# Performance work log

Hardware: AMD Instinct MI355X
Metric: run time of the kernel (lower is better)

Reference implementation:

```python
import jax, jax.numpy as jnp
import numpy as np

E = 16      # num_experts
H = 1024    # hidden_size
O = 1       # output_size
B = 4096    # batch
K = 2       # top-k (hard-coded in module)


def setup_inputs() -> dict:
    key = jax.random.key(0)
    ks = jax.random.split(key, 7)
    s_h = 1.0 / np.sqrt(H)
    inp = {
        "embeddings": jax.random.normal(ks[0], (B, H), dtype=jnp.float32),
        "router_w": jax.random.uniform(ks[1], (H, E), jnp.float32, -s_h, s_h),
        "router_b": jax.random.uniform(ks[2], (E,), jnp.float32, -s_h, s_h),
        "w1": jax.random.uniform(ks[3], (E, H, H), jnp.float32, -s_h, s_h),
        "b1": jax.random.uniform(ks[4], (E, H), jnp.float32, -s_h, s_h),
        "w2": jax.random.uniform(ks[5], (E, H, O), jnp.float32, -s_h, s_h),
        "b2": jax.random.uniform(ks[6], (E, O), jnp.float32, -s_h, s_h),
    }
    return inp


def reference(embeddings, router_w, router_b, w1, b1, w2, b2):
    # Router: top-2 experts per token, softmax over the 2 selected logits.
    logits = embeddings @ router_w + router_b                 # [B, E]
    top_vals, top_idx = jax.lax.top_k(logits, K)              # [B, K]
    top_w = jax.nn.softmax(top_vals, axis=-1)                 # [B, K]

    # Per-expert combine weight: w_e[b] = sum_k top_w[b,k] * (top_idx[b,k]==e)
    onehot = (top_idx[:, :, None] == jnp.arange(E)[None, None, :])  # [B, K, E]
    comb = jnp.einsum('bk,bke->eb', top_w, onehot.astype(top_w.dtype))  # [E, B]

    # Dense per-expert 2-layer MLP (small fixed E); masked-weighted combine
    # reproduces the gather/scatter-add exactly.
    h = jax.nn.relu(jnp.einsum('bh,ehd->ebd', embeddings, w1) + b1[:, None, :])  # [E, B, H]
    out = jnp.einsum('ebd,edo->ebo', h, w2) + b2[:, None, :]                      # [E, B, O]
    prediction = jnp.einsum('eb,ebo->bo', comb, out)                              # [B, O]
    return prediction
```

## Files before the change

kernel.cpp:

```cpp
#include <hip/hip_runtime.h>
#include <hip/hip_bf16.h>
#include <stdint.h>

#define E_EXP 16
#define H_DIM 1024
#define B_TOK 4096
#define BK 64
#define WBM 64
#define WBN 64
#define NSLOT 16
#define KS 16
#define KC 64
#define RTM 128
#define RSTRIDE (KC + 4)

typedef short bf16x8 __attribute__((ext_vector_type(8)));
typedef float f32x4 __attribute__((ext_vector_type(4)));

__device__ __forceinline__ unsigned short f2bf(float x) {
  union { float f; unsigned u; } v; v.f = x;
  unsigned r = v.u + 0x7FFFu + ((v.u >> 16) & 1u);
  return (unsigned short)(r >> 16);
}

__device__ __forceinline__ void gload_lds16(const void* g, void* l) {
  __builtin_amdgcn_global_load_lds(
      (const __attribute__((address_space(1))) void*)g,
      (__attribute__((address_space(3))) void*)l, 16, 0, 0);
}

__global__ __launch_bounds__(256) void k_prep(
    const float* __restrict__ emb, const float* __restrict__ rw,
    const float* __restrict__ w1, unsigned short* __restrict__ emb_bf,
    float* __restrict__ part, unsigned short* __restrict__ w1t,
    int* __restrict__ counts)
{
  __shared__ __align__(16) char smem[RTM * RSTRIDE * 4 + KC * E_EXP * 4];
  const int tid = threadIdx.x;

  if (blockIdx.x == 0 && tid < E_EXP) counts[tid] = 0;

  if (blockIdx.x < 512) {
    float* embL = (float*)smem;
    float* rwL  = (float*)(smem + RTM * RSTRIDE * 4);
    const int t0 = (blockIdx.x & 31) * RTM;
    const int ks = blockIdx.x >> 5;

#pragma unroll
    for (int it = 0; it < 8; ++it) {
      const int i = tid + 256 * it;
      const int row = i >> 4;
      const int c4 = i & 15;
      const size_t goff = (size_t)(t0 + row) * H_DIM + ks * KC + c4 * 4;
      const f32x4 v = *(const f32x4*)(emb + goff);
      ushort4 o;
      o.x = f2bf(v[0]); o.y = f2bf(v[1]); o.z = f2bf(v[2]); o.w = f2bf(v[3]);
      *(ushort4*)(emb_bf + goff) = o;
      *(f32x4*)(embL + row * RSTRIDE + c4 * 4) = v;
    }
    {
      const f32x4 v = *(const f32x4*)(rw + (size_t)ks * (KC * E_EXP) + tid * 4);
      *(f32x4*)(rwL + tid * 4) = v;
    }
    __syncthreads();

    const int w = tid >> 6, lane = tid & 63;
    const int tg = lane & 15, eg = lane >> 4;
    const int ta = w * 32 + tg, tb = ta + 16;

    f32x4 accA = {0.f, 0.f, 0.f, 0.f};
    f32x4 accB = {0.f, 0.f, 0.f, 0.f};
#pragma unroll
    for (int k4 = 0; k4 < KC / 4; ++k4) {
      const f32x4 e0 = *(const f32x4*)(embL + ta * RSTRIDE + k4 * 4);
      const f32x4 e1 = *(const f32x4*)(embL + tb * RSTRIDE + k4 * 4);
#pragma unroll
      for (int h = 0; h < 4; ++h) {
        const f32x4 r = *(const f32x4*)(rwL + (k4 * 4 + h) * E_EXP + eg * 4);
        accA += e0[h] * r;
        accB += e1[h] * r;
      }
    }
    *(f32x4*)(part + ((size_t)ks * B_TOK + t0 + ta) * E_EXP + eg * 4) = accA;
    *(f32x4*)(part + ((size_t)ks * B_TOK + t0 + tb) * E_EXP + eg * 4) = accB;
  } else {
    typedef unsigned short TileT[65];
    TileT* tile = (TileT*)smem;
    const int wb = blockIdx.x - 512;
    const int e  = wb >> 8;
    const int ht = (wb >> 4) & 15;
    const int dt = wb & 15;
    const float* src = w1 + ((size_t)e * H_DIM + ht * 64) * H_DIM + dt * 64;
    const int tr = tid >> 4;
    const int tc = tid & 15;
#pragma unroll
    for (int i = 0; i < 4; ++i) {
      const int r = tr + i * 16;
      const float4 v = *(const float4*)(src + (size_t)r * H_DIM + tc * 4);
      tile[r][tc * 4 + 0] = f2bf(v.x);
      tile[r][tc * 4 + 1] = f2bf(v.y);
      tile[r][tc * 4 + 2] = f2bf(v.z);
      tile[r][tc * 4 + 3] = f2bf(v.w);
    }
    __syncthreads();
    unsigned short* dst = w1t + ((size_t)e * H_DIM + dt * 64) * H_DIM + ht * 64;
    const int wr = tid >> 3;
    const int wc = tid & 7;
#pragma unroll
    for (int i = 0; i < 2; ++i) {
      const int r = wr + i * 32;
      ushort4 t0, t1;
      t0.x = tile[wc * 8 + 0][r]; t0.y = tile[wc * 8 + 1][r];
      t0.z = tile[wc * 8 + 2][r]; t0.w = tile[wc * 8 + 3][r];
      t1.x = tile[wc * 8 + 4][r]; t1.y = tile[wc * 8 + 5][r];
      t1.z = tile[wc * 8 + 6][r]; t1.w = tile[wc * 8 + 7][r];
      *(ushort4*)(dst + (size_t)r * H_DIM + wc * 8) = t0;
      *(ushort4*)(dst + (size_t)r * H_DIM + wc * 8 + 4) = t1;
    }
  }
}

__global__ __launch_bounds__(256) void k_router_select(
    const float* __restrict__ part, const float* __restrict__ rb,
    int* __restrict__ counts, int* __restrict__ lists,
    int4* __restrict__ meta, float2* __restrict__ wts)
{
  __shared__ int lcnt[E_EXP];
  __shared__ int base[E_EXP];
  const int tid = threadIdx.x;
  const int t = blockIdx.x * 256 + tid;
  if (tid < E_EXP) lcnt[tid] = 0;

  float lg[16];
#pragma unroll
  for (int q = 0; q < 4; ++q) {
    const f32x4 b = *(const f32x4*)(rb + q * 4);
    lg[q * 4 + 0] = b[0]; lg[q * 4 + 1] = b[1];
    lg[q * 4 + 2] = b[2]; lg[q * 4 + 3] = b[3];
  }
#pragma unroll
  for (int s = 0; s < KS; ++s) {
#pragma unroll
    for (int q = 0; q < 4; ++q) {
      const f32x4 v = *(const f32x4*)(part + ((size_t)s * B_TOK + t) * E_EXP + q * 4);
      lg[q * 4 + 0] += v[0]; lg[q * 4 + 1] += v[1];
      lg[q * 4 + 2] += v[2]; lg[q * 4 + 3] += v[3];
    }
  }

  float best = -1e30f; int b0 = 0;
#pragma unroll
  for (int e = 0; e < 16; ++e)
    if (lg[e] > best) { best = lg[e]; b0 = e; }
  float best2 = -1e30f; int b1i = 0;
#pragma unroll
  for (int e = 0; e < 16; ++e)
    if (e != b0 && lg[e] > best2) { best2 = lg[e]; b1i = e; }

  __syncthreads();
  const int l0 = atomicAdd(&lcnt[b0], 1);
  const int l1 = atomicAdd(&lcnt[b1i], 1);
  __syncthreads();
  if (tid < E_EXP) base[tid] = atomicAdd(&counts[tid], lcnt[tid]);
  __syncthreads();

  const int p0 = base[b0] + l0;
  const int p1 = base[b1i] + l1;
  lists[b0 * B_TOK + p0] = t;
  lists[b1i * B_TOK + p1] = t;
  meta[t] = make_int4(b0, b1i, p0, p1);
  const float e1v = expf(best2 - best);
  const float w0 = 1.f / (1.f + e1v);
  wts[t] = make_float2(w0, e1v * w0);
}

__global__ __launch_bounds__(64) void k_moe_gemm(
    const unsigned short* __restrict__ emb_bf,
    const unsigned short* __restrict__ w1t,
    const float* __restrict__ b1, const float* __restrict__ w2,
    const int* __restrict__ counts, const int* __restrict__ lists,
    float* __restrict__ outbuf)
{
  const int bid = blockIdx.x;
  const int xcd = bid & 7;
  const int j = bid >> 3;
  const int e  = xcd + 8 * (j >> 8);
  const int r  = j & 255;
  const int nb = r >> 4;
  const int mbg = r & 15;
  const int cnt = counts[e];

  __shared__ unsigned short lA[WBM * BK];
  __shared__ unsigned short lB[WBN * BK];

  const int lane = threadIdx.x;
  const int scb = ((lane & 7) * 16) ^ ((lane >> 3) << 4);
  const int lr = lane & 15, lg = lane >> 4;

  const unsigned short* w1tb = w1t + ((size_t)e * H_DIM + nb * WBN) * H_DIM;
  const float* b1e = b1 + (size_t)e * H_DIM + nb * WBN;
  const float* w2e = w2 + (size_t)e * H_DIM + nb * WBN;

  const unsigned short* bSrc[8];
#pragma unroll
  for (int i = 0; i < 8; ++i) {
    const int n = i * 8 + (lane >> 3);
    bSrc[i] = w1tb + (size_t)n * H_DIM + (scb >> 1);
  }

  for (int mb = mbg; mb * WBM < cnt; mb += 16) {
    const int base = mb * WBM;

    const unsigned short* aSrc[8];
#pragma unroll
    for (int i = 0; i < 8; ++i) {
      const int p = base + i * 8 + (lane >> 3);
      const int tok = lists[e * B_TOK + (p < cnt ? p : 0)];
      aSrc[i] = emb_bf + (size_t)tok * H_DIM + (scb >> 1);
    }

    f32x4 acc[4][4];
#pragma unroll
    for (int m = 0; m < 4; ++m)
#pragma unroll
      for (int n = 0; n < 4; ++n) acc[m][n] = (f32x4){0.f, 0.f, 0.f, 0.f};

#pragma unroll 1
    for (int k0 = 0; k0 < H_DIM; k0 += BK) {
      asm volatile("s_waitcnt lgkmcnt(0)" ::: "memory");
      __builtin_amdgcn_sched_barrier(0);
#pragma unroll
      for (int i = 0; i < 8; ++i)
        gload_lds16(aSrc[i] + k0, (char*)lA + i * 1024);
#pragma unroll
      for (int i = 0; i < 8; ++i)
        gload_lds16(bSrc[i] + k0, (char*)lB + i * 1024);
      asm volatile("s_waitcnt vmcnt(0)" ::: "memory");
      __builtin_amdgcn_sched_barrier(0);

#pragma unroll
      for (int kk = 0; kk < 2; ++kk) {
        const int kb = kk * 64 + lg * 16;
        bf16x8 af[4], bfr[4];
#pragma unroll
        for (int m = 0; m < 4; ++m) {
          const int row = m * 16 + lr;
          af[m] = *(const bf16x8*)((const char*)lA + row * 128 + (kb ^ ((row & 7) << 4)));
        }
#pragma unroll
        for (int n = 0; n < 4; ++n) {
          const int row = n * 16 + lr;
          bfr[n] = *(const bf16x8*)((const char*)lB + row * 128 + (kb ^ ((row & 7) << 4)));
        }
        __builtin_amdgcn_s_setprio(1);
#pragma unroll
        for (int m = 0; m < 4; ++m)
#pragma unroll
          for (int n = 0; n < 4; ++n)
            acc[m][n] = __builtin_amdgcn_mfma_f32_16x16x32_bf16(af[m], bfr[n], acc[m][n], 0, 0, 0);
        __builtin_amdgcn_s_setprio(0);
      }
    }

    float rs[4][4];
#pragma unroll
    for (int m = 0; m < 4; ++m)
#pragma unroll
      for (int r4 = 0; r4 < 4; ++r4) rs[m][r4] = 0.f;

#pragma unroll
    for (int n = 0; n < 4; ++n) {
      const int d = n * 16 + lr;
      const float bb = b1e[d];
      const float ww = w2e[d];
#pragma unroll
      for (int m = 0; m < 4; ++m)
#pragma unroll
        for (int r4 = 0; r4 < 4; ++r4) {
          float v = acc[m][n][r4] + bb;
          v = fmaxf(v, 0.f);
          rs[m][r4] = fmaf(v, ww, rs[m][r4]);
        }
    }
#pragma unroll
    for (int mask = 8; mask >= 1; mask >>= 1) {
#pragma unroll
      for (int m = 0; m < 4; ++m)
#pragma unroll
        for (int r4 = 0; r4 < 4; ++r4) rs[m][r4] += __shfl_xor(rs[m][r4], mask, 64);
    }

    if (lr == 0) {
      float* ob = outbuf + ((size_t)nb * E_EXP + e) * B_TOK + base;
#pragma unroll
      for (int m = 0; m < 4; ++m)
#pragma unroll
        for (int r4 = 0; r4 < 4; ++r4)
          ob[m * 16 + lg * 4 + r4] = rs[m][r4];
    }
  }
}

__global__ __launch_bounds__(256) void k_combine(
    const int4* __restrict__ meta, const float2* __restrict__ wts,
    const float* __restrict__ outbuf, const float* __restrict__ b2,
    float* __restrict__ out)
{
  const int t = blockIdx.x * 256 + threadIdx.x;
  if (t >= B_TOK) return;
  const int4 m = meta[t];
  const float2 w = wts[t];
  float o0 = b2[m.x], o1 = b2[m.y];
#pragma unroll
  for (int s = 0; s < NSLOT; ++s) {
    o0 += outbuf[((size_t)s * E_EXP + m.x) * B_TOK + m.z];
    o1 += outbuf[((size_t)s * E_EXP + m.y) * B_TOK + m.w];
  }
  out[t] = w.x * o0 + w.y * o1;
}

extern "C" void kernel_launch(void* const* d_in, const int* in_sizes, int n_in,
                              void* d_out, int out_size, void* d_ws, size_t ws_size,
                              hipStream_t stream)
{
  const float* emb = (const float*)d_in[0];
  const float* rw  = (const float*)d_in[1];
  const float* rb  = (const float*)d_in[2];
  const float* w1  = (const float*)d_in[3];
  const float* b1  = (const float*)d_in[4];
  const float* w2  = (const float*)d_in[5];
  const float* b2  = (const float*)d_in[6];
  float* out = (float*)d_out;

  char* ws = (char*)d_ws;
  size_t cur = 0;
  auto alloc = [&](size_t bytes) -> void* {
    void* p = ws + cur;
    cur += (bytes + 255) & ~(size_t)255;
    return p;
  };
  int*            counts = (int*)alloc(64);
  int4*           meta   = (int4*)alloc((size_t)B_TOK * 16);
  float2*         wts    = (float2*)alloc((size_t)B_TOK * 8);
  int*            lists  = (int*)alloc((size_t)E_EXP * B_TOK * 4);
  float*          outbuf = (float*)alloc((size_t)NSLOT * E_EXP * B_TOK * 4);
  float*          part   = (float*)alloc((size_t)KS * B_TOK * E_EXP * 4);
  unsigned short* emb_bf = (unsigned short*)alloc((size_t)B_TOK * H_DIM * 2);
  unsigned short* w1t    = (unsigned short*)alloc((size_t)E_EXP * H_DIM * H_DIM * 2);

  k_prep<<<dim3(512 + 4096), 256, 0, stream>>>(emb, rw, w1, emb_bf, part, w1t, counts);
  k_router_select<<<B_TOK / 256, 256, 0, stream>>>(part, rb, counts, lists, meta, wts);
  k_moe_gemm<<<dim3(4096), 64, 0, stream>>>(emb_bf, w1t, b1, w2, counts, lists, outbuf);
  k_combine<<<B_TOK / 256, 256, 0, stream>>>(meta, wts, outbuf, b2, out);
}
```

Baseline: 76.96 us.

## Split K across two waves per block with LDS reduction in MoE GEMM

```diff
diff --git a/kernel.cpp b/kernel.cpp
--- a/kernel.cpp
+++ b/kernel.cpp
@@ -174,7 +174,7 @@
   wts[t] = make_float2(w0, e1v * w0);
 }
 
-__global__ __launch_bounds__(64) void k_moe_gemm(
+__global__ __launch_bounds__(128) void k_moe_gemm(
     const unsigned short* __restrict__ emb_bf,
     const unsigned short* __restrict__ w1t,
     const float* __restrict__ b1, const float* __restrict__ w2,
@@ -184,20 +184,27 @@
   const int bid = blockIdx.x;
   const int xcd = bid & 7;
   const int j = bid >> 3;
-  const int e  = xcd + 8 * (j >> 8);
-  const int r  = j & 255;
-  const int nb = r >> 4;
-  const int mbg = r & 15;
+  const int e  = xcd + 8 * (j >> 7);
+  const int r  = j & 127;
+  const int nb = r >> 3;
+  const int mbg = r & 7;
   const int cnt = counts[e];
 
-  __shared__ unsigned short lA[WBM * BK];
-  __shared__ unsigned short lB[WBN * BK];
-
-  const int lane = threadIdx.x;
+  __shared__ __align__(16) char smem[32768];
+
+  const int tid = threadIdx.x;
+  const int w = tid >> 6;
+  const int lane = tid & 63;
+  char* myA = smem + w * 16384;
+  char* myB = myA + 8192;
+  float* accL = (float*)smem;
+
   const int scb = ((lane & 7) * 16) ^ ((lane >> 3) << 4);
   const int lr = lane & 15, lg = lane >> 4;
-
-  const unsigned short* w1tb = w1t + ((size_t)e * H_DIM + nb * WBN) * H_DIM;
+  const int kb0 = w * (H_DIM / 2);
+
+  const unsigned short* w1tb =
+      w1t + ((size_t)e * H_DIM + nb * WBN) * H_DIM + kb0;
   const float* b1e = b1 + (size_t)e * H_DIM + nb * WBN;
   const float* w2e = w2 + (size_t)e * H_DIM + nb * WBN;
 
@@ -208,7 +215,7 @@
     bSrc[i] = w1tb + (size_t)n * H_DIM + (scb >> 1);
   }
 
-  for (int mb = mbg; mb * WBM < cnt; mb += 16) {
+  for (int mb = mbg; mb * WBM < cnt; mb += 8) {
     const int base = mb * WBM;
 
     const unsigned short* aSrc[8];
@@ -216,7 +223,7 @@
     for (int i = 0; i < 8; ++i) {
       const int p = base + i * 8 + (lane >> 3);
       const int tok = lists[e * B_TOK + (p < cnt ? p : 0)];
-      aSrc[i] = emb_bf + (size_t)tok * H_DIM + (scb >> 1);
+      aSrc[i] = emb_bf + (size_t)tok * H_DIM + kb0 + (scb >> 1);
     }
 
     f32x4 acc[4][4];
@@ -226,15 +233,15 @@
       for (int n = 0; n < 4; ++n) acc[m][n] = (f32x4){0.f, 0.f, 0.f, 0.f};
 
 #pragma unroll 1
-    for (int k0 = 0; k0 < H_DIM; k0 += BK) {
+    for (int k0 = 0; k0 < H_DIM / 2; k0 += BK) {
       asm volatile("s_waitcnt lgkmcnt(0)" ::: "memory");
       __builtin_amdgcn_sched_barrier(0);
 #pragma unroll
       for (int i = 0; i < 8; ++i)
-        gload_lds16(aSrc[i] + k0, (char*)lA + i * 1024);
+        gload_lds16(aSrc[i] + k0, myA + i * 1024);
 #pragma unroll
       for (int i = 0; i < 8; ++i)
-        gload_lds16(bSrc[i] + k0, (char*)lB + i * 1024);
+        gload_lds16(bSrc[i] + k0, myB + i * 1024);
       asm volatile("s_waitcnt vmcnt(0)" ::: "memory");
       __builtin_amdgcn_sched_barrier(0);
 
@@ -245,12 +252,12 @@
 #pragma unroll
         for (int m = 0; m < 4; ++m) {
           const int row = m * 16 + lr;
-          af[m] = *(const bf16x8*)((const char*)lA + row * 128 + (kb ^ ((row & 7) << 4)));
+          af[m] = *(const bf16x8*)(myA + row * 128 + (kb ^ ((row & 7) << 4)));
         }
 #pragma unroll
         for (int n = 0; n < 4; ++n) {
           const int row = n * 16 + lr;
-          bfr[n] = *(const bf16x8*)((const char*)lB + row * 128 + (kb ^ ((row & 7) << 4)));
+          bfr[n] = *(const bf16x8*)(myB + row * 128 + (kb ^ ((row & 7) << 4)));
         }
         __builtin_amdgcn_s_setprio(1);
 #pragma unroll
@@ -262,42 +269,55 @@
       }
     }
 
-    float rs[4][4];
-#pragma unroll
-    for (int m = 0; m < 4; ++m)
-#pragma unroll
-      for (int r4 = 0; r4 < 4; ++r4) rs[m][r4] = 0.f;
-
-#pragma unroll
-    for (int n = 0; n < 4; ++n) {
-      const int d = n * 16 + lr;
-      const float bb = b1e[d];
-      const float ww = w2e[d];
+    __syncthreads();
+    if (w == 1) {
+#pragma unroll
+      for (int n = 0; n < 4; ++n)
+#pragma unroll
+        for (int m = 0; m < 4; ++m)
+          *(f32x4*)(accL + (size_t)(n * 16 + lr) * 68 + m * 16 + lg * 4) = acc[m][n];
+    }
+    __syncthreads();
+    if (w == 0) {
+      float rs[4][4];
 #pragma unroll
       for (int m = 0; m < 4; ++m)
 #pragma unroll
-        for (int r4 = 0; r4 < 4; ++r4) {
-          float v = acc[m][n][r4] + bb;
-          v = fmaxf(v, 0.f);
-          rs[m][r4] = fmaf(v, ww, rs[m][r4]);
+        for (int r4 = 0; r4 < 4; ++r4) rs[m][r4] = 0.f;
+
+#pragma unroll
+      for (int n = 0; n < 4; ++n) {
+        const int d = n * 16 + lr;
+        const float bb = b1e[d];
+        const float ww = w2e[d];
+#pragma unroll
+        for (int m = 0; m < 4; ++m) {
+          const f32x4 oth = *(const f32x4*)(accL + (size_t)d * 68 + m * 16 + lg * 4);
+#pragma unroll
+          for (int r4 = 0; r4 < 4; ++r4) {
+            float v = acc[m][n][r4] + oth[r4] + bb;
+            v = fmaxf(v, 0.f);
+            rs[m][r4] = fmaf(v, ww, rs[m][r4]);
+          }
         }
-    }
-#pragma unroll
-    for (int mask = 8; mask >= 1; mask >>= 1) {
-#pragma unroll
-      for (int m = 0; m < 4; ++m)
-#pragma unroll
-        for (int r4 = 0; r4 < 4; ++r4) rs[m][r4] += __shfl_xor(rs[m][r4], mask, 64);
-    }
-
-    if (lr == 0) {
-      float* ob = outbuf + ((size_t)nb * E_EXP + e) * B_TOK + base;
-#pragma unroll
-      for (int m = 0; m < 4; ++m)
-#pragma unroll
-        for (int r4 = 0; r4 < 4; ++r4)
-          ob[m * 16 + lg * 4 + r4] = rs[m][r4];
-    }
+      }
+#pragma unroll
+      for (int mask = 8; mask >= 1; mask >>= 1) {
+#pragma unroll
+        for (int m = 0; m < 4; ++m)
+#pragma unroll
+          for (int r4 = 0; r4 < 4; ++r4) rs[m][r4] += __shfl_xor(rs[m][r4], mask, 64);
+      }
+      if (lr == 0) {
+        float* ob = outbuf + ((size_t)nb * E_EXP + e) * B_TOK + base;
+#pragma unroll
+        for (int m = 0; m < 4; ++m)
+#pragma unroll
+          for (int r4 = 0; r4 < 4; ++r4)
+            ob[m * 16 + lg * 4 + r4] = rs[m][r4];
+      }
+    }
+    __syncthreads();
   }
 }
 
@@ -350,6 +370,6 @@
 
   k_prep<<<dim3(512 + 4096), 256, 0, stream>>>(emb, rw, w1, emb_bf, part, w1t, counts);
   k_router_select<<<B_TOK / 256, 256, 0, stream>>>(part, rb, counts, lists, meta, wts);
-  k_moe_gemm<<<dim3(4096), 64, 0, stream>>>(emb_bf, w1t, b1, w2, counts, lists, outbuf);
+  k_moe_gemm<<<dim3(2048), 128, 0, stream>>>(emb_bf, w1t, b1, w2, counts, lists, outbuf);
   k_combine<<<B_TOK / 256, 256, 0, stream>>>(meta, wts, outbuf, b2, out);
 }
```

New measurement: 108.1 us. +40.5%, slower.
